# Optimization experiments

Measured on AMD Instinct MI355X. Metric: run time of the kernel, lower is better.

The kernel has to match this reference:

```python
import jax, jax.numpy as jnp
import numpy as np

B, N, IN_F, OUT_F = 8, 2048, 256, 256
ALPHA = 0.2  # LeakyReLU negative slope
NEG_INF = -1e9


def setup_inputs() -> dict:
    key = jax.random.key(0)
    ks = jax.random.split(key, 8)
    h = jax.random.normal(ks[0], (B, N, IN_F), dtype=jnp.float32)
    adj = jax.random.randint(ks[1], (B, N, N), 0, 2, dtype=jnp.int32)
    # xavier-ish scaled params
    W_w = jax.random.normal(ks[2], (OUT_F, IN_F), dtype=jnp.float32) * (1.414 / np.sqrt(IN_F + OUT_F))
    W_b = jnp.zeros((OUT_F,), dtype=jnp.float32)
    ai_w = jax.random.normal(ks[3], (1, OUT_F), dtype=jnp.float32) * (1.414 / np.sqrt(OUT_F + 1))
    ai_b = jnp.zeros((1,), dtype=jnp.float32)
    aj_w = jax.random.normal(ks[4], (1, OUT_F), dtype=jnp.float32) * (1.414 / np.sqrt(OUT_F + 1))
    aj_b = jnp.zeros((1,), dtype=jnp.float32)
    return {"h": h, "adj": adj, "W_w": W_w, "W_b": W_b,
            "ai_w": ai_w, "ai_b": ai_b, "aj_w": aj_w, "aj_b": aj_b}


def reference(h, adj, W_w, W_b, ai_w, ai_b, aj_w, aj_b):
    # Wh: [B, N, F]
    Wh = jnp.einsum('bni,oi->bno', h, W_w) + W_b
    # additive attention scores (pos_embed_dim == 1 so the .view is a transpose)
    Wh1 = jnp.einsum('bnf,of->bno', Wh, ai_w) + ai_b        # [B, N, 1]
    Wh2 = jnp.einsum('bnf,of->bno', Wh, aj_w) + aj_b        # [B, N, 1]
    e = Wh1 + jnp.swapaxes(Wh2, 1, 2)                       # [B, N, N]
    e = jnp.where(e >= 0, e, ALPHA * e)                     # LeakyReLU
    attention = jnp.where(adj > 0, e, NEG_INF)
    attention = jax.nn.softmax(attention, axis=2)
    # dropout: inference mode (training=False) -> identity
    h_hat = jnp.einsum('bnm,bmf->bnf', attention, Wh)
    return jax.nn.elu(h_hat)  # concat=True
```

## Files before the change

### kernel.cpp

```cpp
#include <hip/hip_runtime.h>

typedef __bf16 bf16;
typedef _Float16 f16;
typedef __bf16 bf16x8 __attribute__((ext_vector_type(8)));
typedef _Float16 f16x8 __attribute__((ext_vector_type(8)));
typedef float  f32x4  __attribute__((ext_vector_type(4)));

#define B_  8
#define N_  2048
#define F_  256
#define NTOK (B_ * N_)
static constexpr float LOG2E = 1.44269504088896f;

__device__ __forceinline__ int detect_bf16(const void* h) {
    const unsigned* hw = (const unsigned*)h;
    unsigned w = hw[threadIdx.x & 63];
    unsigned ex = (w >> 7) & 0xFFu;
    unsigned long long b = __ballot(ex > 100u && ex < 150u);
    return __popcll(b) >= 40;
}

__device__ __forceinline__ float ldf(const void* p, int i, int isb) {
    return isb ? (float)((const bf16*)p)[i] : ((const float*)p)[i];
}

__device__ __forceinline__ bf16x8 cvt8(const float* p) {
    float4 a = *(const float4*)p;
    float4 b = *(const float4*)(p + 4);
    bf16x8 r;
    r[0]=(bf16)a.x; r[1]=(bf16)a.y; r[2]=(bf16)a.z; r[3]=(bf16)a.w;
    r[4]=(bf16)b.x; r[5]=(bf16)b.y; r[6]=(bf16)b.z; r[7]=(bf16)b.w;
    return r;
}

__device__ __forceinline__ size_t wht2_idx(int b, int f, int n) {
    int jc = n >> 6;
    int slot = ((n >> 3) & 7) ^ (f & 7);
    return (((size_t)(b * 32 + jc) * F_ + f) << 6) + (slot << 3) + (n & 7);
}

__global__ __launch_bounds__(256)
void k_wht(const void* __restrict__ hv, const void* __restrict__ Wv,
           const void* __restrict__ Wbv, const void* __restrict__ ai_wv,
           const void* __restrict__ ai_bv, const void* __restrict__ aj_wv,
           const void* __restrict__ aj_bv, bf16* __restrict__ WhT2,
           unsigned* __restrict__ adjw) {
    int isb = detect_bf16(hv);
    int ttile = blockIdx.x;
    int fg = threadIdx.x >> 6;
    int lane = threadIdx.x & 63;
    int T0 = ttile * 16;
    int m = lane & 15, quad = lane >> 4;

    f32x4 acc[4];
#pragma unroll
    for (int ft = 0; ft < 4; ++ft) acc[ft] = (f32x4){0.f, 0.f, 0.f, 0.f};

    if (isb) {
        const bf16* hp = (const bf16*)hv + (size_t)(T0 + m) * F_ + quad * 8;
        const bf16* wp = (const bf16*)Wv + (size_t)(fg * 64 + m) * F_ + quad * 8;
#pragma unroll
        for (int kk = 0; kk < F_; kk += 32) {
            bf16x8 hf = *(const bf16x8*)(hp + kk);
#pragma unroll
            for (int ft = 0; ft < 4; ++ft) {
                bf16x8 wf = *(const bf16x8*)(wp + (size_t)ft * 16 * F_ + kk);
                acc[ft] = __builtin_amdgcn_mfma_f32_16x16x32_bf16(wf, hf, acc[ft], 0, 0, 0);
            }
        }
    } else {
        const float* hp = (const float*)hv + (size_t)(T0 + m) * F_ + quad * 8;
        const float* wp = (const float*)Wv + (size_t)(fg * 64 + m) * F_ + quad * 8;
#pragma unroll
        for (int kk = 0; kk < F_; kk += 32) {
            bf16x8 hf = cvt8(hp + kk);
#pragma unroll
            for (int ft = 0; ft < 4; ++ft) {
                bf16x8 wf = cvt8(wp + (size_t)ft * 16 * F_ + kk);
                acc[ft] = __builtin_amdgcn_mfma_f32_16x16x32_bf16(wf, hf, acc[ft], 0, 0, 0);
            }
        }
    }
    int token = T0 + m;
    int b = token >> 11, n = token & (N_ - 1);
    float s_p = 0.f, t_p = 0.f;
#pragma unroll
    for (int ft = 0; ft < 4; ++ft)
#pragma unroll
        for (int r = 0; r < 4; ++r) {
            int f = fg * 64 + ft * 16 + quad * 4 + r;
            float v = acc[ft][r] + ldf(Wbv, f, isb);
            bf16 vb = (bf16)v;
            WhT2[wht2_idx(b, f, n)] = vb;
            float vr = (float)vb;
            s_p += vr * ldf(ai_wv, f, isb);
            t_p += vr * ldf(aj_wv, f, isb);
        }
    s_p += __shfl_down(s_p, 32, 64); s_p += __shfl_down(s_p, 16, 64);
    t_p += __shfl_down(t_p, 32, 64); t_p += __shfl_down(t_p, 16, 64);
    __shared__ float sred[4][16], tred[4][16];
    if (lane < 16) { sred[fg][lane] = s_p; tred[fg][lane] = t_p; }
    __syncthreads();
    if (threadIdx.x < 16) {
        int tid = threadIdx.x;
        int tok = T0 + tid;
        float ss = (sred[0][tid] + sred[1][tid] + sred[2][tid] + sred[3][tid]
                    + ldf(ai_bv, 0, isb)) * LOG2E;
        float tt = (tred[0][tid] + tred[1][tid] + tred[2][tid] + tred[3][tid]
                    + ldf(aj_bv, 0, isb)) * LOG2E;
        f16 th = (f16)tt, sh = (f16)ss;
        unsigned short tu, su;
        __builtin_memcpy(&tu, &th, 2);
        __builtin_memcpy(&su, &sh, 2);
        unsigned w0 = adjw[tok];
        adjw[tok] = (w0 & 0xFFFFu) | ((unsigned)tu << 16);
        unsigned w1 = adjw[NTOK + tok];
        adjw[NTOK + tok] = (w1 & 0xFFFFu) | ((unsigned)su << 16);
    }
}

__global__ __launch_bounds__(256)
void k_attn(const unsigned* __restrict__ adjw, const bf16* __restrict__ WhT2,
            const void* __restrict__ hv, void* __restrict__ outv) {
    int isb = detect_bf16(hv);
    int bid = blockIdx.x;
    int b = bid >> 6, itile = bid & 63, i0 = itile * 32;
    int tid = threadIdx.x;
    int w = tid >> 6, lane = tid & 63, m = lane & 15, q = lane >> 4;
    int jh = w & 1, fh = w >> 1;

    __shared__ __align__(16) char smem[33280];
    unsigned long long* pack64 = (unsigned long long*)smem;
    f16*   tLDS = (f16*)(smem + 8448);
    float* red  = (float*)smem;
    __shared__ float lLDS[2][32];

#pragma unroll
    for (int k = 0; k < 8; ++k) {
        int idx = k * 256 + tid;
        unsigned wv = adjw[b * N_ + idx];
        unsigned short us = (unsigned short)(wv >> 16);
        f16 tv; __builtin_memcpy(&tv, &us, 2);
        tLDS[idx] = tv;
    }
    float s2i0, s2i1;
    {
        unsigned sw0 = adjw[NTOK + b * N_ + i0 + m];
        unsigned sw1 = adjw[NTOK + b * N_ + i0 + 16 + m];
        unsigned short u0 = (unsigned short)(sw0 >> 16);
        unsigned short u1 = (unsigned short)(sw1 >> 16);
        f16 h0, h1;
        __builtin_memcpy(&h0, &u0, 2); __builtin_memcpy(&h1, &u1, 2);
        s2i0 = (float)h0; s2i1 = (float)h1;
    }
#pragma unroll
    for (int k = 0; k < 4; ++k) {
        int id = tid * 4 + k;
        int prow = id >> 5, pc = id & 31;
        const unsigned* src = adjw + ((size_t)(b * N_ + i0 + prow)) * N_ + pc * 64;
        unsigned long long bits = 0;
#pragma unroll
        for (int w8 = 0; w8 < 16; ++w8) {
            uint4 a = *(const uint4*)(src + w8 * 4);
            bits |= (unsigned long long)((a.x & 1u) | ((a.y & 1u) << 1) |
                                         ((a.z & 1u) << 2) | ((a.w & 1u) << 3))
                    << (w8 * 4);
        }
        pack64[prow * 33 + pc] = bits;
    }
    __syncthreads();

    bf16x8 ones;
#pragma unroll
    for (int k = 0; k < 8; ++k) ones[k] = (bf16)1.0f;

    f32x4 acc0[8], acc1[8];
#pragma unroll
    for (int ft = 0; ft < 8; ++ft) {
        acc0[ft] = (f32x4){0.f, 0.f, 0.f, 0.f};
        acc1[ft] = (f32x4){0.f, 0.f, 0.f, 0.f};
    }
    f32x4 acc_l0 = {0.f, 0.f, 0.f, 0.f}, acc_l1 = {0.f, 0.f, 0.f, 0.f};

    int psl = (jh * 4 + q) ^ (m & 7);
    const size_t tilestep = (size_t)F_ * 64;
    const bf16* btile = WhT2 + (size_t)(b * 32) * tilestep +
                        (size_t)(fh * 128) * 64 + m * 64 + psl * 8;
    int byi = jh * 4 + q;

    for (int c = 0; c < 32; ++c) {
        unsigned long long pb0 = pack64[m * 33 + c];
        unsigned long long pb1 = pack64[(16 + m) * 33 + c];
        unsigned bits0 = (unsigned)(pb0 >> (byi * 8)) & 0xFFu;
        unsigned bits1 = (unsigned)(pb1 >> (byi * 8)) & 0xFFu;
        f16x8 tv = *(const f16x8*)(tLDS + c * 64 + jh * 32 + q * 8);

        bf16x8 af0, af1;
#pragma unroll
        for (int qq = 0; qq < 8; ++qq) {
            float tvf = (float)tv[qq];
            float x0 = s2i0 + tvf, x1 = s2i1 + tvf;
            x0 = fmaxf(x0, 0.2f * x0);
            x1 = fmaxf(x1, 0.2f * x1);
            x0 = fminf(fmaxf(x0, -120.f), 60.f);
            x1 = fminf(fmaxf(x1, -120.f), 60.f);
            float p0 = ((bits0 >> qq) & 1u) ? __builtin_amdgcn_exp2f(x0) : 0.f;
            float p1 = ((bits1 >> qq) & 1u) ? __builtin_amdgcn_exp2f(x1) : 0.f;
            af0[qq] = (bf16)p0;
            af1[qq] = (bf16)p1;
        }
        if (fh == 0) {
            acc_l0 = __builtin_amdgcn_mfma_f32_16x16x32_bf16(af0, ones, acc_l0, 0, 0, 0);
            acc_l1 = __builtin_amdgcn_mfma_f32_16x16x32_bf16(af1, ones, acc_l1, 0, 0, 0);
        }
        const bf16* bp = btile + (size_t)c * tilestep;
#pragma unroll
        for (int ft = 0; ft < 8; ++ft) {
            bf16x8 bfr = *(const bf16x8*)(bp + ft * 1024);
            acc0[ft] = __builtin_amdgcn_mfma_f32_16x16x32_bf16(af0, bfr, acc0[ft], 0, 0, 0);
            acc1[ft] = __builtin_amdgcn_mfma_f32_16x16x32_bf16(af1, bfr, acc1[ft], 0, 0, 0);
        }
        if ((c & 3) == 3) __syncthreads();
    }

    __syncthreads();
    if (fh == 0 && m == 0) {
#pragma unroll
        for (int r = 0; r < 4; ++r) {
            lLDS[jh][q * 4 + r]      = acc_l0[r];
            lLDS[jh][16 + q * 4 + r] = acc_l1[r];
        }
    }
    if (jh == 1) {
#pragma unroll
        for (int r = 0; r < 4; ++r) {
            int r0 = q * 4 + r, r1 = 16 + q * 4 + r;
#pragma unroll
            for (int ft = 0; ft < 8; ++ft) {
                red[r0 * 260 + fh * 128 + ft * 16 + m] = acc0[ft][r];
                red[r1 * 260 + fh * 128 + ft * 16 + m] = acc1[ft][r];
            }
        }
    }
    __syncthreads();
    if (jh == 0) {
#pragma unroll
        for (int mt = 0; mt < 2; ++mt) {
#pragma unroll
            for (int r = 0; r < 4; ++r) {
                int row = mt * 16 + q * 4 + r;
                float lf = lLDS[0][row] + lLDS[1][row];
                float rl = (lf > 0.f) ? (1.f / lf) : 0.f;
                size_t ob = ((size_t)b * N_ + i0 + row) * F_;
#pragma unroll
                for (int ft = 0; ft < 8; ++ft) {
                    int f = fh * 128 + ft * 16 + m;
                    float v = (mt ? acc1[ft][r] : acc0[ft][r]) + red[row * 260 + f];
                    v *= rl;
                    v = (v > 0.f) ? v : (__builtin_amdgcn_exp2f(v * LOG2E) - 1.f);
                    if (isb) ((bf16*)outv)[ob + f] = (bf16)v;
                    else     ((float*)outv)[ob + f] = v;
                }
            }
        }
    }
}

extern "C" void kernel_launch(void* const* d_in, const int* in_sizes, int n_in,
                              void* d_out, int out_size, void* d_ws, size_t ws_size,
                              hipStream_t stream) {
    (void)in_sizes; (void)n_in; (void)out_size; (void)ws_size;
    const void* h    = d_in[0];
    unsigned*   adjw = (unsigned*)d_in[1];
    const void* W_w  = d_in[2];
    const void* W_b  = d_in[3];
    const void* ai_w = d_in[4];
    const void* ai_b = d_in[5];
    const void* aj_w = d_in[6];
    const void* aj_b = d_in[7];

    bf16* WhT2 = (bf16*)d_ws;

    k_wht <<<dim3(1024), dim3(256), 0, stream>>>(h, W_w, W_b, ai_w, ai_b,
                                                 aj_w, aj_b, WhT2, adjw);
    k_attn<<<dim3(512),  dim3(256), 0, stream>>>(adjw, WhT2, h, d_out);
}
```

Baseline: 316.1 us.

## Double-buffer WhT tiles in LDS via async global_load_lds prefetch

The per-chunk Wh^T tiles are now staged into two 32 KB LDS buffers with asynchronous global-to-LDS loads. The next chunk is prefetched while the current chunk's MFMAs run, and the B fragments are read from LDS instead of straight from global memory. This hides global load latency and removes repeated global reads of the same tile by different waves. In exchange, LDS use per block grows from about 33 KB to about 78 KB, which can lower occupancy, and a barrier now runs every iteration instead of every fourth.

```diff
diff --git a/kernel.cpp b/kernel.cpp
--- a/kernel.cpp
+++ b/kernel.cpp
@@ -119,6 +119,19 @@
     }
 }
 
+__device__ __forceinline__ void stageB(const bf16* tile, char* dst,
+                                       int w, int lane) {
+#pragma unroll
+    for (int r = 0; r < 8; ++r) {
+        int off = (w * 8 + r) * 1024;
+        const bf16* g = tile + off / 2 + lane * 8;
+        __builtin_amdgcn_global_load_lds(
+            (const __attribute__((address_space(1))) unsigned*)g,
+            (__attribute__((address_space(3))) unsigned*)(dst + off),
+            16, 0, 0);
+    }
+}
+
 __global__ __launch_bounds__(256)
 void k_attn(const unsigned* __restrict__ adjw, const bf16* __restrict__ WhT2,
             const void* __restrict__ hv, void* __restrict__ outv) {
@@ -129,9 +142,11 @@
     int w = tid >> 6, lane = tid & 63, m = lane & 15, q = lane >> 4;
     int jh = w & 1, fh = w >> 1;
 
-    __shared__ __align__(16) char smem[33280];
-    unsigned long long* pack64 = (unsigned long long*)smem;
-    f16*   tLDS = (f16*)(smem + 8448);
+    __shared__ __align__(16) char smem[78080];
+    char* Bbuf0 = smem;
+    char* Bbuf1 = smem + 32768;
+    unsigned long long* pack64 = (unsigned long long*)(smem + 65536);
+    f16*   tLDS = (f16*)(smem + 65536 + 8448);
     float* red  = (float*)smem;
     __shared__ float lLDS[2][32];
 
@@ -168,6 +183,9 @@
         }
         pack64[prow * 33 + pc] = bits;
     }
+    const size_t tilestep = (size_t)F_ * 64;
+    const bf16* btiles = WhT2 + (size_t)(b * 32) * tilestep;
+    stageB(btiles, Bbuf0, w, lane);
     __syncthreads();
 
     bf16x8 ones;
@@ -183,12 +201,14 @@
     f32x4 acc_l0 = {0.f, 0.f, 0.f, 0.f}, acc_l1 = {0.f, 0.f, 0.f, 0.f};
 
     int psl = (jh * 4 + q) ^ (m & 7);
-    const size_t tilestep = (size_t)F_ * 64;
-    const bf16* btile = WhT2 + (size_t)(b * 32) * tilestep +
-                        (size_t)(fh * 128) * 64 + m * 64 + psl * 8;
     int byi = jh * 4 + q;
 
     for (int c = 0; c < 32; ++c) {
+        char* Bcur = (c & 1) ? Bbuf1 : Bbuf0;
+        if (c < 31)
+            stageB(btiles + (size_t)(c + 1) * tilestep,
+                   (c & 1) ? Bbuf0 : Bbuf1, w, lane);
+
         unsigned long long pb0 = pack64[m * 33 + c];
         unsigned long long pb1 = pack64[(16 + m) * 33 + c];
         unsigned bits0 = (unsigned)(pb0 >> (byi * 8)) & 0xFFu;
@@ -213,17 +233,16 @@
             acc_l0 = __builtin_amdgcn_mfma_f32_16x16x32_bf16(af0, ones, acc_l0, 0, 0, 0);
             acc_l1 = __builtin_amdgcn_mfma_f32_16x16x32_bf16(af1, ones, acc_l1, 0, 0, 0);
         }
-        const bf16* bp = btile + (size_t)c * tilestep;
 #pragma unroll
         for (int ft = 0; ft < 8; ++ft) {
-            bf16x8 bfr = *(const bf16x8*)(bp + ft * 1024);
+            int fr = fh * 128 + ft * 16 + m;
+            bf16x8 bfr = *(const bf16x8*)(Bcur + fr * 128 + psl * 16);
             acc0[ft] = __builtin_amdgcn_mfma_f32_16x16x32_bf16(af0, bfr, acc0[ft], 0, 0, 0);
             acc1[ft] = __builtin_amdgcn_mfma_f32_16x16x32_bf16(af1, bfr, acc1[ft], 0, 0, 0);
         }
-        if ((c & 3) == 3) __syncthreads();
-    }
-
-    __syncthreads();
+        __syncthreads();
+    }
+
     if (fh == 0 && m == 0) {
 #pragma unroll
         for (int r = 0; r < 4; ++r) {
```

Measured after the change: 301.1 us. 4.7% less time.
